# Performance work log

Hardware: AMD Instinct MI355X
Metric: run time of the kernel (lower is better)

Reference implementation:

```python
import jax, jax.numpy as jnp
import numpy as np

NJ, IC = 17, 128          # njoints, inner channels
NB = 19                    # basic blocks after the first (20 total)
DILS = (3, 6, 12, 18, 24)  # dilations of the 5 offset / deform-conv branches
KK = 9                     # 3x3 kernel taps


def conv2d(x, w, pad, dil=1):
    # NCHW conv, stride 1, symmetric padding, optional dilation, no bias
    return jax.lax.conv_general_dilated(
        x, w, (1, 1), [(pad, pad), (pad, pad)], rhs_dilation=(dil, dil),
        dimension_numbers=('NCHW', 'OIHW', 'NCHW'))


def bn(x, scale, shift):
    # inference-mode BatchNorm folded to per-channel affine
    return x * scale[None, :, None, None] + shift[None, :, None, None]


def basic_block(h, w1, s1, b1, w2, s2, b2):
    out = jax.nn.relu(bn(conv2d(h, w1, 1), s1, b1))
    out = bn(conv2d(out, w2, 1), s2, b2)
    return jax.nn.relu(out + h)


def deform_conv(x, offsets, w, dil):
    # x: [B,C,H,W] with C == deformable_groups (1 channel per group)
    # offsets: [B, C*2*KK, H, W] in (dy, dx) pairs per tap per group
    # w: [C, C, 3, 3]; stride 1, padding = dil so output is HxW
    B, C, H, W = x.shape
    off = offsets.reshape(B, C, KK, 2, H, W)
    dy, dx = off[:, :, :, 0], off[:, :, :, 1]                    # [B,C,9,H,W]
    ky, kx = jnp.meshgrid(jnp.arange(3), jnp.arange(3), indexing='ij')
    base_y = ((ky.reshape(-1) - 1) * dil).astype(jnp.float32)    # [9]
    base_x = ((kx.reshape(-1) - 1) * dil).astype(jnp.float32)
    py = dy + base_y[None, None, :, None, None] + jnp.arange(H, dtype=jnp.float32)[:, None]
    px = dx + base_x[None, None, :, None, None] + jnp.arange(W, dtype=jnp.float32)[None, :]
    y0 = jnp.floor(py); x0 = jnp.floor(px)
    wy = py - y0; wx = px - x0
    y0i = y0.astype(jnp.int32); x0i = x0.astype(jnp.int32)
    img = x.reshape(B, C, H * W)

    def gather(yi, xi):
        valid = (yi >= 0) & (yi < H) & (xi >= 0) & (xi < W)
        idx = jnp.clip(yi, 0, H - 1) * W + jnp.clip(xi, 0, W - 1)
        v = jnp.take_along_axis(img, idx.reshape(B, C, -1), axis=2)
        return v.reshape(B, C, KK, H, W) * valid

    v00 = gather(y0i, x0i); v01 = gather(y0i, x0i + 1)
    v10 = gather(y0i + 1, x0i); v11 = gather(y0i + 1, x0i + 1)
    samp = (v00 * (1 - wy) * (1 - wx) + v01 * (1 - wy) * wx +
            v10 * wy * (1 - wx) + v11 * wy * wx)                 # [B,C,9,H,W]
    return jnp.einsum('oik,bikhw->bohw', w.reshape(w.shape[0], C, KK), samp)


def setup_inputs() -> dict:
    key = jax.random.key(0)
    ks = iter(jax.random.split(key, 40))
    B, H, W = 2, 96, 72

    def wgt(shape, fan_in):
        return jax.random.normal(next(ks), shape, jnp.float32) * np.float32(np.sqrt(2.0 / fan_in))

    def bnp(c, stacked=None):
        sh = (stacked, c) if stacked else (c,)
        s = jax.random.uniform(next(ks), sh, jnp.float32, 0.5, 1.5)
        b = jax.random.normal(next(ks), sh, jnp.float32) * 0.1
        return s, b

    x = jax.random.normal(next(ks), (B, NJ, H, W), jnp.float32)
    y = jax.random.normal(next(ks), (B, NJ, H, W), jnp.float32)
    blk0_w1 = wgt((IC, NJ, 3, 3), NJ * 9)
    blk0_s1, blk0_b1 = bnp(IC)
    blk0_w2 = wgt((IC, IC, 3, 3), IC * 9)
    blk0_s2, blk0_b2 = bnp(IC)
    blk0_wd = wgt((IC, NJ, 1, 1), NJ)
    blk0_sd, blk0_bd = bnp(IC)
    blk_w1 = wgt((NB, IC, IC, 3, 3), IC * 9)
    blk_s1, blk_b1 = bnp(IC, NB)
    blk_w2 = wgt((NB, IC, IC, 3, 3), IC * 9)
    blk_s2, blk_b2 = bnp(IC, NB)
    off_w = jax.random.normal(next(ks), (5, NJ * 2 * KK, IC, 3, 3), jnp.float32) * 0.01
    dc_w = wgt((5, NJ, NJ, 3, 3), NJ * 9)
    return dict(x=x, y=y,
                blk0_w1=blk0_w1, blk0_s1=blk0_s1, blk0_b1=blk0_b1,
                blk0_w2=blk0_w2, blk0_s2=blk0_s2, blk0_b2=blk0_b2,
                blk0_wd=blk0_wd, blk0_sd=blk0_sd, blk0_bd=blk0_bd,
                blk_w1=blk_w1, blk_s1=blk_s1, blk_b1=blk_b1,
                blk_w2=blk_w2, blk_s2=blk_s2, blk_b2=blk_b2,
                off_w=off_w, dc_w=dc_w)


def reference(x, y, blk0_w1, blk0_s1, blk0_b1, blk0_w2, blk0_s2, blk0_b2,
              blk0_wd, blk0_sd, blk0_bd, blk_w1, blk_s1, blk_b1,
              blk_w2, blk_s2, blk_b2, off_w, dc_w):
    diff = y - x
    # first BasicBlock (with 1x1 downsample projecting njoints -> 128)
    res = bn(conv2d(diff, blk0_wd, 0), blk0_sd, blk0_bd)
    out = jax.nn.relu(bn(conv2d(diff, blk0_w1, 1), blk0_s1, blk0_b1))
    out = bn(conv2d(out, blk0_w2, 1), blk0_s2, blk0_b2)
    feat = jax.nn.relu(out + res)

    def step(h, p):
        w1, s1, b1, w2, s2, b2 = p
        return basic_block(h, w1, s1, b1, w2, s2, b2), None

    feat, _ = jax.lax.scan(step, feat, (blk_w1, blk_s1, blk_b1, blk_w2, blk_s2, blk_b2))

    warped = jnp.zeros_like(x)
    for i, dil in enumerate(DILS):
        off = conv2d(feat, off_w[i], dil, dil)          # [B, 306, H, W]
        warped = warped + deform_conv(x, off, dc_w[i], dil)
    return 0.2 * warped
```

## Files before the change

kernel.cpp:

```cpp
#include <hip/hip_runtime.h>
#include <hip/hip_bf16.h>

#define NPX 6912
typedef unsigned long long u64;
typedef int i32x4 __attribute__((ext_vector_type(4)));

__device__ __forceinline__ int ea_from_bits(u64 bits){
    double m = __longlong_as_double((long long)bits);
    if (!(m > 0.0)) return 0;
    return ilogb(m) + 1;
}
__device__ __forceinline__ void digits4(double a, int sh, int& d0, int& d1, int& d2, int& d3){
    long long q = __double2ll_rn(ldexp(a, sh));
    d3 = (int)(((q + 128) & 255) - 128); q = (q - d3) >> 8;
    d2 = (int)(((q + 128) & 255) - 128); q = (q - d2) >> 8;
    d1 = (int)(((q + 128) & 255) - 128);
    d0 = (int)((q - d1) >> 8);
}
__device__ __forceinline__ int xcd_swz(int bid, int nwg){
    return (bid & 7) * (nwg >> 3) + (bid >> 3);
}

__global__ __launch_bounds__(256) void diff_kd(const float* __restrict__ x,
    const float* __restrict__ y, double* __restrict__ d, int n,
    u64* maxbuf, int slot){
    int i = blockIdx.x*256 + threadIdx.x;
    double m = 0.0;
    if (i < n){ double v = (double)y[i] - (double)x[i]; d[i] = v; m = fabs(v); }
    #pragma unroll
    for (int o=32;o;o>>=1) m = fmax(m, __shfl_down(m,o));
    __shared__ double W[4];
    if ((threadIdx.x&63)==0) W[threadIdx.x>>6]=m;
    __syncthreads();
    if (threadIdx.x==0){
        m = fmax(fmax(W[0],W[1]),fmax(W[2],W[3]));
        atomicMax(maxbuf+slot,(u64)__double_as_longlong(m));
    }
}

__global__ __launch_bounds__(256) void conv1x1_d(const double* __restrict__ in,
    const float* __restrict__ wgt, const float* __restrict__ scale,
    const float* __restrict__ shift, double* __restrict__ out){
    __shared__ float Ws[17*128];
    const int t = threadIdx.x;
    for (int e=t; e<17*128; e+=256){
        int ic = e >> 7, oc = e & 127;
        Ws[e] = wgt[oc*17 + ic];
    }
    __syncthreads();
    const int pxl = t & 31, ocg = t >> 5;
    const int p = blockIdx.x*32 + pxl;
    const int b = p / NPX, pi = p - b*NPX;
    double acc[16];
    #pragma unroll
    for (int j=0;j<16;j++) acc[j]=0.0;
    const double* inb = in + (size_t)b*17*NPX + pi;
    #pragma unroll
    for (int ic=0;ic<17;ic++){
        const double a = inb[(size_t)ic*NPX];
        #pragma unroll
        for (int j=0;j<16;j++) acc[j] = fma(a, (double)Ws[(ic<<7)+(ocg<<4)+j], acc[j]);
    }
    #pragma unroll
    for (int j=0;j<16;j++){
        const int oc = (ocg<<4)+j;
        out[((size_t)b*128+oc)*NPX + pi] = fma(acc[j], (double)scale[oc], (double)shift[oc]);
    }
}

__global__ __launch_bounds__(256) void adecomp_k(const double* __restrict__ src,
    signed char* __restrict__ dst, const u64* __restrict__ maxbuf, int slot,
    int PS, int PW, int PB)
{
    __shared__ signed char L[4][8][128];
    const int t = threadIdx.x;
    const int b = blockIdx.x / 864, px0 = (blockIdx.x % 864) * 8;
    const int sh = 30 - ea_from_bits(maxbuf[slot]);
    const int tp = t & 7, tc = t >> 3;
    #pragma unroll
    for (int i=0;i<4;i++){
        const int c = tc + i*32;
        double a = src[((size_t)b*128 + c)*NPX + px0 + tp];
        int d0,d1,d2,d3; digits4(a, sh, d0,d1,d2,d3);
        L[0][tp][c] = (signed char)d0;
        L[1][tp][c] = (signed char)d1;
        L[2][tp][c] = (signed char)d2;
        L[3][tp][c] = (signed char)d3;
    }
    __syncthreads();
    const int l = t >> 6, px = (t >> 3) & 7, chunk = t & 7;
    const int pix = px0 + px, yy = pix/72, xx = pix - yy*72;
    const size_t po = ((size_t)(l*2+b)*PS + (size_t)(yy+PB)*PW + (xx+PB))*128 + chunk*16;
    *(uint4*)(dst+po) = *(const uint4*)(&L[l][px][chunk*16]);
}

__global__ __launch_bounds__(256) void adecomp17_k(const double* __restrict__ src,
    signed char* __restrict__ dst, const u64* __restrict__ maxbuf, int slot)
{
    __shared__ signed char L[4][16][64];
    const int t = threadIdx.x;
    const int b = blockIdx.x / 432, px0 = (blockIdx.x % 432) * 16;
    const int sh = 30 - ea_from_bits(maxbuf[slot]);
    uint4 z = {0,0,0,0};
    *(uint4*)(((signed char*)L) + t*16) = z;
    __syncthreads();
    const int tp = t & 15, tc = t >> 4;
    #pragma unroll
    for (int i=0;i<2;i++){
        const int c = tc + i*16;
        if (c < 17){
            double a = src[((size_t)b*17 + c)*NPX + px0 + tp];
            int d0,d1,d2,d3; digits4(a, sh, d0,d1,d2,d3);
            L[0][tp][c] = (signed char)d0;
            L[1][tp][c] = (signed char)d1;
            L[2][tp][c] = (signed char)d2;
            L[3][tp][c] = (signed char)d3;
        }
    }
    __syncthreads();
    const int l = t >> 6, wpx = (t >> 2) & 15, chunk = t & 3;
    const int pix = px0 + wpx, yy = pix/72, xx = pix - yy*72;
    const size_t po = ((size_t)(l*2+b)*7448 + (size_t)(yy+1)*76 + (xx+1))*64 + chunk*16;
    *(uint4*)(dst+po) = *(const uint4*)(&L[l][wpx][chunk*16]);
}

__device__ __forceinline__ void wprep_body(const float* src,
    signed char* Bpk, int* Eb, int oc, int t,
    int ocw, int ICw, int ICpad, int OCpad)
{
    const int NW = ICw*9;
    float m = 0.f;
    if (oc < ocw)
        for (int e=t;e<NW;e+=64) m = fmaxf(m, fabsf(src[(size_t)oc*NW+e]));
    #pragma unroll
    for (int o=32;o;o>>=1) m = fmaxf(m, __shfl_down(m,o));
    m = __shfl(m, 0);
    const int Ebv = (m>0.f)?(ilogbf(m)+1):0;
    if (t==0) Eb[oc]=Ebv;
    const int sh = 30 - Ebv;
    const int nc16 = ICpad >> 4;
    const int PERSTEP = 4*32*ICpad;
    const size_t perOt = (size_t)9*PERSTEP;
    const int ot = oc >> 5, o32 = oc & 31;
    const int nchunks = nc16*9;
    for (int mci=t; mci<nchunks; mci+=64){
        const int ic16 = mci % nc16, tap = mci / nc16;
        const int xk = (ICpad==128) ? (ic16 ^ (o32 & 7)) : (ic16 ^ ((o32>>1) & 3));
        __align__(16) signed char dig[4][16];
        #pragma unroll
        for (int j=0;j<16;j++){
            const int ic = ic16*16+j;
            float w = (oc<ocw && ic<ICw) ? src[((size_t)oc*ICw+ic)*9+tap] : 0.f;
            int d0,d1,d2,d3; digits4((double)w, sh, d0,d1,d2,d3);
            dig[0][j]=(signed char)d0;
            dig[1][j]=(signed char)d1;
            dig[2][j]=(signed char)d2;
            dig[3][j]=(signed char)d3;
        }
        const size_t base = (size_t)ot*perOt + (size_t)tap*PERSTEP
                          + (size_t)o32*ICpad + (xk<<4);
        #pragma unroll
        for (int l=0;l<4;l++)
            *(uint4*)(Bpk + base + (size_t)l*32*ICpad) = *(const uint4*)(&dig[l][0]);
    }
}

__global__ __launch_bounds__(64) void wprep_k(const float* __restrict__ wgt,
    signed char* __restrict__ Bpk, int* __restrict__ Eb,
    int ocw, int ICw, int ICpad, int OCpad)
{
    wprep_body(wgt, Bpk, Eb, blockIdx.x, threadIdx.x, ocw, ICw, ICpad, OCpad);
}

__global__ __launch_bounds__(64) void wprep_all(
    const float* __restrict__ b0w1, const float* __restrict__ b0w2,
    const float* __restrict__ bw1, const float* __restrict__ bw2,
    const float* __restrict__ offw,
    signed char* __restrict__ BpkAll, int* __restrict__ EbAll)
{
    const int slot = blockIdx.y;
    const float* src; int ocw, ICw, ICpad, OCpad;
    signed char* Bpk;
    if (slot < 40){
        Bpk = BpkAll + (size_t)slot * 589824;
        ocw = 128; OCpad = 128;
        if (slot == 0){ src=b0w1; ICw=17; ICpad=64; }
        else if (slot == 1){ src=b0w2; ICw=128; ICpad=128; }
        else { int i=(slot-2)>>1; src = (((slot-2)&1)? bw2:bw1) + (size_t)i*147456; ICw=128; ICpad=128; }
    } else {
        Bpk = BpkAll + 40ull*589824 + (size_t)(slot-40)*1474560;
        src = offw + (size_t)(slot-40)*352512; ocw=306; ICw=128; ICpad=128; OCpad=320;
    }
    if ((int)blockIdx.x >= OCpad) return;
    wprep_body(src, Bpk, EbAll + slot*320, blockIdx.x, threadIdx.x, ocw, ICw, ICpad, OCpad);
}

#define MFI(A,B,C) __builtin_amdgcn_mfma_i32_16x16x64_i8(A,B,C,0,0,0)

template<int MODE, int NCC>
__global__ __launch_bounds__(256, 2) void convL(
    const signed char* __restrict__ inL, int PS, int PW, int PB, int dil,
    const signed char* __restrict__ Bpk, const int* __restrict__ Eb,
    int OCw, int OCT,
    const u64* __restrict__ maxbuf, int easlot,
    const float* __restrict__ scale, const float* __restrict__ shift,
    const double* res, void* outp, u64* maxout, int moslot)
{
    constexpr int CC = NCC*64;
    constexpr int NSTEP = 9;
    constexpr int PERSTEP = 4*32*CC;
    constexpr int LSTR = 32*CC;
    __shared__ signed char Bs[2][PERSTEP];
    const int t = threadIdx.x;
    const int w = t >> 6, lane = t & 63;
    const int ocl = lane & 15, rq = lane >> 4;
    const int lb = xcd_swz(blockIdx.x, gridDim.x);
    const int oct = lb % OCT, pxt = lb / OCT;
    const int b = pxt / 54, px0 = (pxt - b*54) * 128 + w*32;
    const int oc0 = oct * 32;

    long long aBase[2];
    #pragma unroll
    for (int mt=0; mt<2; mt++){
        const int px = px0 + mt*16 + ocl;
        const int sy = px/72, sx = px - sy*72;
        aBase[mt] = ((long long)b*PS + (long long)(sy+PB)*PW + (sx+PB))*CC + rq*16;
    }
    const long long pStr = (long long)2*PS*CC;
    const signed char* Bsl = Bpk + (size_t)oct * ((size_t)NSTEP*PERSTEP);

    i32x4 c0[2][2], c1[2][2], c2[2][2], c3[2][2];
    #pragma unroll
    for (int i=0;i<2;i++)
      #pragma unroll
      for (int j=0;j<2;j++){
        c0[i][j]=(i32x4)(0); c1[i][j]=(i32x4)(0);
        c2[i][j]=(i32x4)(0); c3[i][j]=(i32x4)(0);
      }

    const int Ea = ea_from_bits(maxbuf[easlot]);

    auto STAGE = [&](int s, int buf){
        const signed char* src = Bsl + (size_t)s*PERSTEP + w*1024 + (lane<<4);
        #pragma unroll
        for (int j=0;j<PERSTEP/4096;j++)
            __builtin_amdgcn_global_load_lds((const unsigned int*)(src + j*4096),
                                             (unsigned int*)(&Bs[buf][j*4096 + w*1024]), 16, 0, 0);
    };

    STAGE(0, 0);
    __builtin_amdgcn_sched_barrier(0);

    for (int s=0; s<NSTEP; s++){
        if (s == 0)           asm volatile("s_waitcnt vmcnt(0)  lgkmcnt(0)" ::: "memory");
        else if (NCC==2)      asm volatile("s_waitcnt vmcnt(16) lgkmcnt(0)" ::: "memory");
        else                  asm volatile("s_waitcnt vmcnt(8)  lgkmcnt(0)" ::: "memory");
        __builtin_amdgcn_s_barrier();
        __builtin_amdgcn_sched_barrier(0);

        if (s+1 < NSTEP) STAGE(s+1, (s+1)%2);

        const int ty = s/3, tx = s - ty*3;
        const long long dofs = ((long long)(ty-1)*PW + (tx-1)) * dil * CC;
        const signed char* bsb = &Bs[s%2][0];

        i32x4 af[NCC][2][4];
        #pragma unroll
        for (int icc=0; icc<NCC; icc++)
          #pragma unroll
          for (int mt=0; mt<2; mt++)
            #pragma unroll
            for (int l=0;l<4;l++)
                af[icc][mt][l] = *(const i32x4*)(inL + (aBase[mt] + dofs + icc*64 + (long long)l*pStr));

        i32x4 bfr[NCC][2][4];
        #pragma unroll
        for (int icc=0; icc<NCC; icc++)
          #pragma unroll
          for (int nt=0; nt<2; nt++){
            const int o32 = nt*16 + ocl;
            const int xk = (NCC==2) ? ((icc*4+rq) ^ (o32 & 7)) : (rq ^ ((o32>>1) & 3));
            const int off = o32*CC + (xk<<4);
            #pragma unroll
            for (int l=0;l<4;l++)
                bfr[icc][nt][l] = *(const i32x4*)(bsb + l*LSTR + off);
          }

        __builtin_amdgcn_s_setprio(1);
        #pragma unroll
        for (int icc=0; icc<NCC; icc++)
          #pragma unroll
          for (int nt=0; nt<2; nt++)
            #pragma unroll
            for (int mt=0; mt<2; mt++){
              c0[mt][nt]=MFI(af[icc][mt][0],bfr[icc][nt][0],c0[mt][nt]);
              c1[mt][nt]=MFI(af[icc][mt][0],bfr[icc][nt][1],c1[mt][nt]);
              c1[mt][nt]=MFI(af[icc][mt][1],bfr[icc][nt][0],c1[mt][nt]);
              c2[mt][nt]=MFI(af[icc][mt][0],bfr[icc][nt][2],c2[mt][nt]);
              c2[mt][nt]=MFI(af[icc][mt][1],bfr[icc][nt][1],c2[mt][nt]);
              c2[mt][nt]=MFI(af[icc][mt][2],bfr[icc][nt][0],c2[mt][nt]);
              c3[mt][nt]=MFI(af[icc][mt][0],bfr[icc][nt][3],c3[mt][nt]);
              c3[mt][nt]=MFI(af[icc][mt][1],bfr[icc][nt][2],c3[mt][nt]);
              c3[mt][nt]=MFI(af[icc][mt][2],bfr[icc][nt][1],c3[mt][nt]);
              c3[mt][nt]=MFI(af[icc][mt][3],bfr[icc][nt][0],c3[mt][nt]);
            }
        __builtin_amdgcn_s_setprio(0);
    }

    if (MODE != 2){
        double mx = 0.0;
        #pragma unroll
        for (int nt=0;nt<2;nt++){
            const int oc = oc0 + nt*16 + ocl;
            const int ex = Ea + Eb[oc] - 36;
            const double sc = (double)scale[oc], sf = (double)shift[oc];
            #pragma unroll
            for (int mt=0;mt<2;mt++){
                const size_t ob = ((size_t)(b*128+oc))*NPX + px0 + mt*16 + rq*4;
                double4 rv;
                if (MODE==1) rv = *(const double4*)(res+ob);
                double vv[4];
                #pragma unroll
                for (int v=0;v<4;v++){
                    const long long comb = ((long long)c0[mt][nt][v]<<24) + ((long long)c1[mt][nt][v]<<16)
                                         + ((long long)c2[mt][nt][v]<<8)  +  (long long)c3[mt][nt][v];
                    double dv = fma(ldexp((double)comb, ex), sc, sf);
                    if (MODE==1) dv += (&rv.x)[v];
                    dv = dv>0.0 ? dv : 0.0;
                    vv[v]=dv; mx = fmax(mx,dv);
                }
                double4 st = {vv[0],vv[1],vv[2],vv[3]};
                *(double4*)((double*)outp+ob) = st;
            }
        }
        #pragma unroll
        for (int o=32;o;o>>=1) mx = fmax(mx,__shfl_down(mx,o));
        if (lane==0) atomicMax(maxout+moslot,(u64)__double_as_longlong(mx));
    } else {
        #pragma unroll
        for (int nt=0;nt<2;nt++){
            const int oc = oc0 + nt*16 + ocl;
            if (oc < OCw){
                const int ex = Ea + Eb[oc] - 36;
                #pragma unroll
                for (int mt=0;mt<2;mt++){
                    const size_t ob = ((size_t)b*OCw+oc)*NPX + px0 + mt*16 + rq*4;
                    float4 st;
                    #pragma unroll
                    for (int v=0;v<4;v++){
                        const long long comb = ((long long)c0[mt][nt][v]<<24) + ((long long)c1[mt][nt][v]<<16)
                                             + ((long long)c2[mt][nt][v]<<8)  +  (long long)c3[mt][nt][v];
                        (&st.x)[v] = (float)ldexp((double)comb, ex);
                    }
                    *(float4*)((float*)outp+ob) = st;
                }
            }
        }
    }
}

__global__ __launch_bounds__(256) void deform_kd(
    const float* __restrict__ xin, const float* __restrict__ off,
    const float* __restrict__ dcw, float* out, int dil)
{
    __shared__ float Wsm[17*153];
    __shared__ double R[16][16][17];
    const int t = threadIdx.x;
    for (int e=t;e<17*153;e+=256) Wsm[e] = dcw[e];
    __syncthreads();
    const int pxl = t & 15, cg = t >> 4;
    const int p = blockIdx.x*16 + pxl;
    const int b = p / NPX, pi = p - b*NPX;
    const int yy = pi/72, xx = pi - yy*72;
    const float* img = xin + (size_t)b*17*NPX;
    const float* ob  = off + (size_t)b*306*NPX + pi;
    const int cbeg = (cg==0) ? 0 : (cg+1);
    const int cnt  = (cg==0) ? 2 : 1;
    double acc[17];
    #pragma unroll
    for (int o=0;o<17;o++) acc[o]=0.0;
    for (int ci=0; ci<cnt; ci++){
        const int c = cbeg + ci;
        const float* im = img + c*NPX;
        #pragma unroll
        for (int k=0;k<9;k++){
            const double dy = (double)ob[((c*9+k)*2+0)*NPX];
            const double dx = (double)ob[((c*9+k)*2+1)*NPX];
            const double py  = (double)yy + dy + (double)((k/3-1)*dil);
            const double pxd = (double)xx + dx + (double)((k%3-1)*dil);
            const double y0f = floor(py), x0f = floor(pxd);
            const double wy = py - y0f, wx = pxd - x0f;
            const int y0 = (int)fmax(fmin(y0f, 97.0), -2.0);
            const int x0 = (int)fmax(fmin(x0f, 73.0), -2.0);
            const bool yv0 = (y0   >= 0) && (y0   < 96);
            const bool yv1 = (y0+1 >= 0) && (y0+1 < 96);
            const bool xv0 = (x0   >= 0) && (x0   < 72);
            const bool xv1 = (x0+1 >= 0) && (x0+1 < 72);
            const int yc0 = min(max(y0  ,0),95), yc1 = min(max(y0+1,0),95);
            const int xc0 = min(max(x0  ,0),71), xc1 = min(max(x0+1,0),71);
            const double v00 = (yv0&&xv0) ? (double)im[yc0*72+xc0] : 0.0;
            const double v01 = (yv0&&xv1) ? (double)im[yc0*72+xc1] : 0.0;
            const double v10 = (yv1&&xv0) ? (double)im[yc1*72+xc0] : 0.0;
            const double v11 = (yv1&&xv1) ? (double)im[yc1*72+xc1] : 0.0;
            const double s = v00*(1.0-wy)*(1.0-wx) + v01*(1.0-wy)*wx
                           + v10*wy*(1.0-wx)       + v11*wy*wx;
            const int ck = c*9+k;
            #pragma unroll
            for (int o=0;o<17;o++)
                acc[o] = fma((double)Wsm[o*153+ck], s, acc[o]);
        }
    }
    #pragma unroll
    for (int o=0;o<17;o++) R[cg][pxl][o] = acc[o];
    __syncthreads();
    const int og = cg;
    const int obeg = (og==0) ? 0 : (og+1);
    const int ocnt = (og==0) ? 2 : 1;
    for (int oi=0; oi<ocnt; oi++){
        const int o = obeg + oi;
        double s = 0.0;
        #pragma unroll
        for (int g=0; g<16; g++) s += R[g][pxl][o];
        atomicAdd(out + ((size_t)b*17+o)*NPX + pi, (float)(0.2*s));
    }
}

extern "C" void kernel_launch(void* const* d_in, const int* in_sizes, int n_in,
                              void* d_out, int out_size, void* d_ws, size_t ws_size,
                              hipStream_t stream)
{
    const float* x    = (const float*)d_in[0];
    const float* y    = (const float*)d_in[1];
    const float* b0w1 = (const float*)d_in[2];
    const float* b0s1 = (const float*)d_in[3];
    const float* b0b1 = (const float*)d_in[4];
    const float* b0w2 = (const float*)d_in[5];
    const float* b0s2 = (const float*)d_in[6];
    const float* b0b2 = (const float*)d_in[7];
    const float* b0wd = (const float*)d_in[8];
    const float* b0sd = (const float*)d_in[9];
    const float* b0bd = (const float*)d_in[10];
    const float* bw1  = (const float*)d_in[11];
    const float* bs1  = (const float*)d_in[12];
    const float* bb1  = (const float*)d_in[13];
    const float* bw2  = (const float*)d_in[14];
    const float* bs2  = (const float*)d_in[15];
    const float* bb2  = (const float*)d_in[16];
    const float* offw = (const float*)d_in[17];
    const float* dcw  = (const float*)d_in[18];
    float* out = (float*)d_out;

    const size_t BPK_BIG = 40ull*589824 + 5ull*1474560;
    char* P = (char*)d_ws;
    auto nxt = [&](size_t bytes){ char* r = P; P += (bytes + 255) & ~(size_t)255; return r; };
    double* hbuf = (double*)nxt(14155776);
    u64*  maxbuf = (u64*)nxt(512);
    const size_t NEED_BIG = 14155776 + 512 + 57600 + BPK_BIG + 41631744 + 4096;
    const bool big = (ws_size >= NEED_BIG);
    int* EbR = (int*)nxt(big ? 57600 : 1536);
    signed char* BpkR = (signed char*)nxt(big ? BPK_BIG : 1474560);
    char* R0 = nxt(41631744);
    signed char* actL  = (signed char*)R0;
    signed char* diffL = (signed char*)(R0 + 7626752);
    double* diffd = (double*)(R0 + 7626752 + 3813376);
    double* res0  = (double*)(R0 + 7626752 + 3813376 + 1880064);
    double* obuf  = (double*)(R0 + 7626752 + 3813376 + 1880064 + 14155776);
    signed char* bigL = (signed char*)R0;
    float* offb = (float*)(R0 + 17694720);
    const size_t actLB = 7626752, diffLB = 3813376, bigLB = 17694720;

    auto Bp = [&](int slot)->signed char*{
        if (!big) return BpkR;
        return slot < 40 ? BpkR + (size_t)slot*589824
                         : BpkR + 40ull*589824 + (size_t)(slot-40)*1474560;
    };
    auto Ep = [&](int slot)->int*{ return big ? EbR + slot*320 : EbR; };
    auto prep = [&](int slot){
        if (big) return;
        const float* src; int ocw, ICw, ICpad, OCpad;
        if (slot == 0){ src=b0w1; ocw=128; ICw=17; ICpad=64; OCpad=128; }
        else if (slot == 1){ src=b0w2; ocw=128; ICw=128; ICpad=128; OCpad=128; }
        else if (slot < 40){ int i=(slot-2)>>1;
            src = (((slot-2)&1)? bw2:bw1) + (size_t)i*147456;
            ocw=128; ICw=128; ICpad=128; OCpad=128; }
        else { src = offw + (size_t)(slot-40)*352512; ocw=306; ICw=128; ICpad=128; OCpad=320; }
        hipLaunchKernelGGL(wprep_k, dim3(OCpad), dim3(64), 0, stream,
                           src, BpkR, EbR, ocw, ICw, ICpad, OCpad);
    };

    dim3 b256(256);
    hipMemsetAsync(actL, 0, actLB, stream);
    hipMemsetAsync(diffL, 0, diffLB, stream);
    hipMemsetAsync(maxbuf, 0, 512, stream);
    hipMemsetAsync(d_out, 0, (size_t)out_size*sizeof(float), stream);
    if (big)
        hipLaunchKernelGGL(wprep_all, dim3(320,45), dim3(64), 0, stream,
                           b0w1, b0w2, bw1, bw2, offw, BpkR, EbR);

    hipLaunchKernelGGL(diff_kd, dim3(918), b256, 0, stream, x, y, diffd, 235008, maxbuf, 40);
    hipLaunchKernelGGL(conv1x1_d, dim3(432), b256, 0, stream, diffd, b0wd, b0sd, b0bd, res0);
    hipLaunchKernelGGL(adecomp17_k, dim3(864), b256, 0, stream, diffd, diffL, maxbuf, 40);
    prep(0);
    hipLaunchKernelGGL((convL<0,1>), dim3(432), b256, 0, stream,
                       diffL, 7448, 76, 1, 1, Bp(0), Ep(0), 128, 4, maxbuf, 40,
                       b0s1, b0b1, (const double*)nullptr, (void*)obuf, maxbuf, 0);
    hipLaunchKernelGGL(adecomp_k, dim3(1728), b256, 0, stream, obuf, actL, maxbuf, 0, 7448, 76, 1);
    prep(1);
    hipLaunchKernelGGL((convL<1,2>), dim3(432), b256, 0, stream,
                       actL, 7448, 76, 1, 1, Bp(1), Ep(1), 128, 4, maxbuf, 0,
                       b0s2, b0b2, (const double*)res0, (void*)hbuf, maxbuf, 1);
    hipLaunchKernelGGL(adecomp_k, dim3(1728), b256, 0, stream, hbuf, actL, maxbuf, 1, 7448, 76, 1);

    for (int i = 0; i < 19; i++){
        const int sIn = 2*i + 1, sO = 2*i + 2, sH = 2*i + 3;
        prep(2+2*i);
        hipLaunchKernelGGL((convL<0,2>), dim3(432), b256, 0, stream,
                           actL, 7448, 76, 1, 1, Bp(2+2*i), Ep(2+2*i), 128, 4, maxbuf, sIn,
                           bs1 + i*128, bb1 + i*128, (const double*)nullptr,
                           (void*)obuf, maxbuf, sO);
        hipLaunchKernelGGL(adecomp_k, dim3(1728), b256, 0, stream, obuf, actL, maxbuf, sO, 7448, 76, 1);
        prep(3+2*i);
        hipLaunchKernelGGL((convL<1,2>), dim3(432), b256, 0, stream,
                           actL, 7448, 76, 1, 1, Bp(3+2*i), Ep(3+2*i), 128, 4, maxbuf, sO,
                           bs2 + i*128, bb2 + i*128, (const double*)hbuf,
                           (void*)hbuf, maxbuf, sH);
        if (i < 18)
            hipLaunchKernelGGL(adecomp_k, dim3(1728), b256, 0, stream, hbuf, actL, maxbuf, sH, 7448, 76, 1);
    }

    hipMemsetAsync(bigL, 0, bigLB, stream);
    hipLaunchKernelGGL(adecomp_k, dim3(1728), b256, 0, stream, hbuf, bigL, maxbuf, 39, 17280, 120, 24);
    const int dils[5] = {3,6,12,18,24};
    for (int d = 0; d < 5; d++){
        prep(40+d);
        hipLaunchKernelGGL((convL<2,2>), dim3(1080), b256, 0, stream,
                           bigL, 17280, 120, 24, dils[d], Bp(40+d), Ep(40+d), 306, 10, maxbuf, 39,
                           (const float*)nullptr, (const float*)nullptr,
                           (const double*)nullptr, (void*)offb, (u64*)nullptr, 0);
        hipLaunchKernelGGL(deform_kd, dim3(864), b256, 0, stream,
                           x, offb, dcw + (size_t)d*2601, out, dils[d]);
    }
}
```

Baseline: 3.181 ms.

## Batch all five dilation offset convs and deform convs into single launches

Replaces the per-dilation loop of offset-conv plus deform-conv launches with one convLo kernel over all five dilations and one deform_all kernel. convLo uses a 32-output-channel tile with double-buffered LDS staging of weights via global_load_lds, and launch_bounds of 2 for occupancy. The aim is to fill the GPU with more blocks per launch and cut launch and serialization overhead. It needs a larger workspace for five offset buffers and falls back to the old path when the workspace is too small.

New measurement: 3.042 ms. 4.4% less time.

```diff
diff --git a/kernel.cpp b/kernel.cpp
--- a/kernel.cpp
+++ b/kernel.cpp
@@ -359,17 +359,133 @@
     }
 }
 
-__global__ __launch_bounds__(256) void deform_kd(
-    const float* __restrict__ xin, const float* __restrict__ off,
-    const float* __restrict__ dcw, float* out, int dil)
+__global__ __launch_bounds__(256, 2) void convLo(
+    const signed char* __restrict__ inL, int PS, int PW, int PB,
+    const signed char* __restrict__ BpkAll, const int* __restrict__ EbAll,
+    const u64* __restrict__ maxbuf, int easlot, float* __restrict__ outAll)
+{
+    constexpr int CC = 128;
+    constexpr int NSTEP = 9;
+    constexpr int PERSTEP = 4*32*CC;
+    constexpr int LSTR = 32*CC;
+    __shared__ signed char Bs[2][PERSTEP];
+    const int t = threadIdx.x;
+    const int w = t >> 6, lane = t & 63;
+    const int ocl = lane & 15, rq = lane >> 4;
+    const int lb = xcd_swz(blockIdx.x, gridDim.x);
+    const int d = lb / 2160, r = lb - d*2160;
+    const int dil = d ? 6*d : 3;
+    const int oct = r % 10, pxt = r / 10;
+    const int b = pxt / 108, px0 = (pxt - b*108) * 64 + w*16;
+    const int oc0 = oct * 32;
+    const int* Eb = EbAll + d*320;
+    float* outp = outAll + (size_t)d*4230144;
+
+    const int px = px0 + ocl;
+    const int sy = px/72, sx = px - sy*72;
+    const long long aBase = ((long long)b*PS + (long long)(sy+PB)*PW + (sx+PB))*CC + rq*16;
+    const long long pStr = (long long)2*PS*CC;
+    const signed char* Bsl = BpkAll + (size_t)d*1474560 + (size_t)oct * ((size_t)NSTEP*PERSTEP);
+
+    i32x4 c0[2], c1[2], c2[2], c3[2];
+    #pragma unroll
+    for (int j=0;j<2;j++){
+        c0[j]=(i32x4)(0); c1[j]=(i32x4)(0);
+        c2[j]=(i32x4)(0); c3[j]=(i32x4)(0);
+    }
+
+    const int Ea = ea_from_bits(maxbuf[easlot]);
+
+    auto STAGE = [&](int s, int buf){
+        const signed char* src = Bsl + (size_t)s*PERSTEP + w*1024 + (lane<<4);
+        #pragma unroll
+        for (int j=0;j<PERSTEP/4096;j++)
+            __builtin_amdgcn_global_load_lds((const unsigned int*)(src + j*4096),
+                                             (unsigned int*)(&Bs[buf][j*4096 + w*1024]), 16, 0, 0);
+    };
+
+    STAGE(0, 0);
+    __builtin_amdgcn_sched_barrier(0);
+
+    for (int s=0; s<NSTEP; s++){
+        if (s == 0) asm volatile("s_waitcnt vmcnt(0) lgkmcnt(0)" ::: "memory");
+        else        asm volatile("s_waitcnt vmcnt(8) lgkmcnt(0)" ::: "memory");
+        __builtin_amdgcn_s_barrier();
+        __builtin_amdgcn_sched_barrier(0);
+
+        if (s+1 < NSTEP) STAGE(s+1, (s+1)%2);
+
+        const int ty = s/3, tx = s - ty*3;
+        const long long dofs = ((long long)(ty-1)*PW + (tx-1)) * dil * CC;
+        const signed char* bsb = &Bs[s%2][0];
+
+        i32x4 af[2][4];
+        #pragma unroll
+        for (int icc=0; icc<2; icc++)
+          #pragma unroll
+          for (int l=0;l<4;l++)
+            af[icc][l] = *(const i32x4*)(inL + (aBase + dofs + icc*64 + (long long)l*pStr));
+
+        i32x4 bfr[2][2][4];
+        #pragma unroll
+        for (int icc=0; icc<2; icc++)
+          #pragma unroll
+          for (int nt=0; nt<2; nt++){
+            const int o32 = nt*16 + ocl;
+            const int xk = (icc*4+rq) ^ (o32 & 7);
+            const int off = o32*CC + (xk<<4);
+            #pragma unroll
+            for (int l=0;l<4;l++)
+                bfr[icc][nt][l] = *(const i32x4*)(bsb + l*LSTR + off);
+          }
+
+        __builtin_amdgcn_s_setprio(1);
+        #pragma unroll
+        for (int icc=0; icc<2; icc++)
+          #pragma unroll
+          for (int nt=0; nt<2; nt++){
+            c0[nt]=MFI(af[icc][0],bfr[icc][nt][0],c0[nt]);
+            c1[nt]=MFI(af[icc][0],bfr[icc][nt][1],c1[nt]);
+            c1[nt]=MFI(af[icc][1],bfr[icc][nt][0],c1[nt]);
+            c2[nt]=MFI(af[icc][0],bfr[icc][nt][2],c2[nt]);
+            c2[nt]=MFI(af[icc][1],bfr[icc][nt][1],c2[nt]);
+            c2[nt]=MFI(af[icc][2],bfr[icc][nt][0],c2[nt]);
+            c3[nt]=MFI(af[icc][0],bfr[icc][nt][3],c3[nt]);
+            c3[nt]=MFI(af[icc][1],bfr[icc][nt][2],c3[nt]);
+            c3[nt]=MFI(af[icc][2],bfr[icc][nt][1],c3[nt]);
+            c3[nt]=MFI(af[icc][3],bfr[icc][nt][0],c3[nt]);
+          }
+        __builtin_amdgcn_s_setprio(0);
+    }
+
+    #pragma unroll
+    for (int nt=0;nt<2;nt++){
+        const int oc = oc0 + nt*16 + ocl;
+        if (oc < 306){
+            const int ex = Ea + Eb[oc] - 36;
+            const size_t ob = ((size_t)b*306+oc)*NPX + px0 + rq*4;
+            float4 st;
+            #pragma unroll
+            for (int v=0;v<4;v++){
+                const long long comb = ((long long)c0[nt][v]<<24) + ((long long)c1[nt][v]<<16)
+                                     + ((long long)c2[nt][v]<<8)  +  (long long)c3[nt][v];
+                (&st.x)[v] = (float)ldexp((double)comb, ex);
+            }
+            *(float4*)(outp+ob) = st;
+        }
+    }
+}
+
+__device__ __forceinline__ void deform_body(
+    const float* xin, const float* off, const float* dcw, float* out, int dil,
+    int blk, int t)
 {
     __shared__ float Wsm[17*153];
     __shared__ double R[16][16][17];
-    const int t = threadIdx.x;
     for (int e=t;e<17*153;e+=256) Wsm[e] = dcw[e];
     __syncthreads();
     const int pxl = t & 15, cg = t >> 4;
-    const int p = blockIdx.x*16 + pxl;
+    const int p = blk*16 + pxl;
     const int b = p / NPX, pi = p - b*NPX;
     const int yy = pi/72, xx = pi - yy*72;
     const float* img = xin + (size_t)b*17*NPX;
@@ -425,6 +541,23 @@
     }
 }
 
+__global__ __launch_bounds__(256) void deform_kd(
+    const float* __restrict__ xin, const float* __restrict__ off,
+    const float* __restrict__ dcw, float* out, int dil)
+{
+    deform_body(xin, off, dcw, out, dil, blockIdx.x, threadIdx.x);
+}
+
+__global__ __launch_bounds__(256) void deform_all(
+    const float* __restrict__ xin, const float* __restrict__ offAll,
+    const float* __restrict__ dcwAll, float* out)
+{
+    const int d = blockIdx.x / 864, blk = blockIdx.x - d*864;
+    const int dil = d ? 6*d : 3;
+    deform_body(xin, offAll + (size_t)d*4230144, dcwAll + d*2601, out, dil,
+                blk, threadIdx.x);
+}
+
 extern "C" void kernel_launch(void* const* d_in, const int* in_sizes, int n_in,
                               void* d_out, int out_size, void* d_ws, size_t ws_size,
                               hipStream_t stream)
@@ -451,15 +584,19 @@
     float* out = (float*)d_out;
 
     const size_t BPK_BIG = 40ull*589824 + 5ull*1474560;
+    const size_t R0_SER  = 41631744;
+    const size_t R0_FUS  = 17694720 + 5ull*16920576;
     char* P = (char*)d_ws;
     auto nxt = [&](size_t bytes){ char* r = P; P += (bytes + 255) & ~(size_t)255; return r; };
     double* hbuf = (double*)nxt(14155776);
     u64*  maxbuf = (u64*)nxt(512);
-    const size_t NEED_BIG = 14155776 + 512 + 57600 + BPK_BIG + 41631744 + 4096;
-    const bool big = (ws_size >= NEED_BIG);
+    const size_t NEED_BIG = 14155776 + 512 + 57600 + BPK_BIG + R0_SER + 4096;
+    const size_t NEED_FUS = 14155776 + 512 + 57600 + BPK_BIG + (R0_FUS > R0_SER ? R0_FUS : R0_SER) + 8192;
+    const bool big   = (ws_size >= NEED_BIG);
+    const bool fused = (ws_size >= NEED_FUS) && big;
     int* EbR = (int*)nxt(big ? 57600 : 1536);
     signed char* BpkR = (signed char*)nxt(big ? BPK_BIG : 1474560);
-    char* R0 = nxt(41631744);
+    char* R0 = nxt(fused ? (R0_FUS > R0_SER ? R0_FUS : R0_SER) : R0_SER);
     signed char* actL  = (signed char*)R0;
     signed char* diffL = (signed char*)(R0 + 7626752);
     double* diffd = (double*)(R0 + 7626752 + 3813376);
@@ -530,14 +667,20 @@
 
     hipMemsetAsync(bigL, 0, bigLB, stream);
     hipLaunchKernelGGL(adecomp_k, dim3(1728), b256, 0, stream, hbuf, bigL, maxbuf, 39, 17280, 120, 24);
-    const int dils[5] = {3,6,12,18,24};
-    for (int d = 0; d < 5; d++){
-        prep(40+d);
-        hipLaunchKernelGGL((convL<2,2>), dim3(1080), b256, 0, stream,
-                           bigL, 17280, 120, 24, dils[d], Bp(40+d), Ep(40+d), 306, 10, maxbuf, 39,
-                           (const float*)nullptr, (const float*)nullptr,
-                           (const double*)nullptr, (void*)offb, (u64*)nullptr, 0);
-        hipLaunchKernelGGL(deform_kd, dim3(864), b256, 0, stream,
-                           x, offb, dcw + (size_t)d*2601, out, dils[d]);
-    }
-}
+    if (fused){
+        hipLaunchKernelGGL(convLo, dim3(10800), b256, 0, stream,
+                           bigL, 17280, 120, 24, Bp(40), Ep(40), maxbuf, 39, offb);
+        hipLaunchKernelGGL(deform_all, dim3(4320), b256, 0, stream, x, offb, dcw, out);
+    } else {
+        const int dils[5] = {3,6,12,18,24};
+        for (int d = 0; d < 5; d++){
+            prep(40+d);
+            hipLaunchKernelGGL((convL<2,2>), dim3(1080), b256, 0, stream,
+                               bigL, 17280, 120, 24, dils[d], Bp(40+d), Ep(40+d), 306, 10, maxbuf, 39,
+                               (const float*)nullptr, (const float*)nullptr,
+                               (const double*)nullptr, (void*)offb, (u64*)nullptr, 0);
+            hipLaunchKernelGGL(deform_kd, dim3(864), b256, 0, stream,
+                               x, offb, dcw + (size_t)d*2601, out, dils[d]);
+        }
+    }
+}
```
